# Kernel tuning notes

Measured on AMD Instinct MI355X. Metric: run time of the kernel, lower is better.

## Reference

```python
import jax, jax.numpy as jnp
import numpy as np

B, L, D = 8, 8192, 1024
M = L // 4  # target_ratio=4 -> exactly L/4 boundaries per batch row (enforced in setup_inputs)


@jax.custom_vjp
def ste(x):
    # Forward: ones_like(x). Backward: pass gradient straight through.
    return jnp.ones_like(x)

def _ste_fwd(x):
    return jnp.ones_like(x), None

def _ste_bwd(_, g):
    return (g,)

ste.defvjp(_ste_fwd, _ste_bwd)


def _ema_combine(c1, c2):
    # Linear recurrence h = a*h_prev + b as an associative op (matches the
    # Hillis-Steele doubling scan in the torch source exactly).
    a1, b1 = c1
    a2, b2 = c2
    return (a1 * a2, a2[..., None] * b1 + b2)


def setup_inputs() -> dict:
    key = jax.random.key(0)
    k1, k2, k3, k4, k5 = jax.random.split(key, 5)
    x = jax.random.normal(k1, (B, L, D), jnp.float32)
    residual = jax.random.normal(k2, (B, L, D), jnp.float32)
    prob = jax.random.uniform(k3, (B, L), jnp.float32)
    # exactly M=L//4 True positions per row (random locations) -> static M
    r = jax.random.uniform(k4, (B, L))
    sel = jnp.argsort(r, axis=1)[:, :M]
    token_mask = jnp.zeros((B, L), bool).at[jnp.arange(B)[:, None], sel].set(True)
    state = jax.random.normal(k5, (B, D), jnp.float32)
    return {"x": x, "residual": residual, "prob": prob,
            "token_mask": token_mask, "state": state}


def reference(x, residual, prob, token_mask, state):
    # ---- Tokenizer: compact selected positions to the front (stable order) ----
    counts = token_mask.sum(axis=1)                       # (B,)
    order = jnp.argsort(~token_mask, axis=1)[:, :M]       # stable: True positions first, in order
    chunked = jnp.take_along_axis(x, order[:, :, None], axis=1)      # (B, M, D)
    chunk_probs = jnp.take_along_axis(prob, order, axis=1)           # (B, M)
    valid = jnp.arange(M)[None, :] < counts[:, None]                  # (B, M)
    chunk_probs = chunk_probs * valid                     # padded slots -> 0 (new_zeros semantics)

    # ---- EMA scan over compacted chunks ----
    decay = jnp.clip(1.0 - chunk_probs, 0.0, 1.0)         # (B, M)
    b = (1.0 - decay)[..., None] * chunked                # (B, M, D)
    b = b.at[:, 0].add(decay[:, 0, None] * state)         # fold initial state into b[0]
    _, ema = jax.lax.associative_scan(_ema_combine, (decay, b), axis=1)
    ema = ema * valid[..., None]

    # ---- DeTokenizer: scatter-expand back to (B, L, D) ----
    chunk_idx = jnp.cumsum(token_mask.astype(jnp.int32), axis=1) - 1  # (B, L)
    valid_pos = chunk_idx >= 0
    ci = jnp.clip(chunk_idx, 0, M - 1)
    long_states = jnp.take_along_axis(ema, ci[:, :, None], axis=1)    # (B, L, D)
    long_states = long_states * valid_pos[..., None]

    coef = ste(jnp.maximum(1.0 - prob, prob))             # forward: ones; bwd: STE
    long_states = long_states * coef[..., None]

    output = residual + long_states                       # (B, L, D)

    # new_state = last valid EMA value per batch (or carried-over state if empty)
    last = jnp.clip(counts - 1, 0, M - 1)
    new_state = jnp.take_along_axis(ema, last[:, None, None], axis=1)[:, 0]
    new_state = jnp.where((counts > 0)[:, None], new_state, state)
    return output, new_state
```

## Files before the change

kernel.cpp:

```cpp
#include <hip/hip_runtime.h>
#include <stdint.h>
#include <stddef.h>

#define B_ 8
#define L_ 8192
#define D_ 1024
#define M_ 2048
#define D4_ (D_/4)
#define TROWS_ 256
#define NTILE_ (L_/TROWS_)
#define NBLK_ (B_*NTILE_)

typedef float f4 __attribute__((ext_vector_type(4)));

#define OFF_FLAG   ((size_t)0)
#define OFF_A      ((size_t)256)
#define OFF_CNT    (OFF_A    + (size_t)NBLK_*4)
#define OFF_LIVE   (OFF_CNT  + (size_t)NBLK_*4)
#define OFF_EZ     (OFF_LIVE + (size_t)NBLK_*4)
#define OFF_HINIT  (OFF_EZ   + (size_t)NBLK_*D_*4)
#define WS_TOTAL   (OFF_HINIT + (size_t)NBLK_*D_*4)

__global__ __launch_bounds__(256)
void segend_kernel(const f4* __restrict__ x4,
                   const float* __restrict__ prob,
                   const void* __restrict__ mask_raw,
                   f4* __restrict__ ez4,
                   float* __restrict__ Aseg,
                   int* __restrict__ cnt,
                   int* __restrict__ u8out) {
    const int blk = blockIdx.x;
    const int b = blk >> 5;
    const int k = blk & (NTILE_ - 1);
    const int t = threadIdx.x;
    const int l0 = k * TROWS_;

    __shared__ int   u8flag;
    __shared__ int   wsum[4];
    __shared__ int   pl[TROWS_ + 2];
    __shared__ float dl[TROWS_ + 2];

    if (t == 0) u8flag = 0;
    __syncthreads();
    {
        const uint32_t* mu = (const uint32_t*)mask_raw;
        uint32_t orv = 0;
        #pragma unroll
        for (int j = 0; j < 8; j++) orv |= mu[t * 8 + j];
        if (orv > 1u) atomicOr(&u8flag, 1);
    }
    pl[t] = L_; dl[t] = 1.0f;
    if (t < 2) { pl[TROWS_ + t] = L_; dl[TROWS_ + t] = 1.0f; }
    __syncthreads();
    const bool u8 = (u8flag != 0);
    if (blk == 0 && t == 0) *u8out = u8 ? 1 : 0;

    const int gl = b * L_ + l0 + t;
    const int mv = u8 ? (((const uint8_t*)mask_raw)[gl] ? 1 : 0)
                      : (((const int*)mask_raw)[gl] ? 1 : 0);
    const float dv = fminf(fmaxf(1.0f - prob[gl], 0.0f), 1.0f);
    const int lane = t & 63, wid = t >> 6;
    int v = mv;
    #pragma unroll
    for (int off = 1; off < 64; off <<= 1) {
        int nn = __shfl_up(v, off, 64);
        if (lane >= off) v += nn;
    }
    if (lane == 63) wsum[wid] = v;
    __syncthreads();
    int acc = 0;
    #pragma unroll
    for (int w = 0; w < 4; w++) if (w < wid) acc += wsum[w];
    const int n = wsum[0] + wsum[1] + wsum[2] + wsum[3];
    const int excl = (v - mv) + acc;
    if (mv) { pl[excl] = l0 + t; dl[excl] = dv; }
    __syncthreads();

    f4 h = (f4)(0.0f);
    float A = 1.0f;
    const f4* xrow = x4 + (size_t)b * L_ * D4_;
    for (int g = 0; g < n; g += 8) {
        f4    xv[8];
        float dd[8];
        #pragma unroll
        for (int j = 0; j < 8; j++) {
            const int mm = g + j;
            const int mc = (mm < n) ? mm : 0;
            dd[j] = (mm < n) ? dl[mc] : 1.0f;
            xv[j] = xrow[(size_t)pl[mc] * D4_ + t];
        }
        #pragma unroll
        for (int j = 0; j < 8; j++) {
            h = dd[j] * h + (1.0f - dd[j]) * xv[j];
            A *= dd[j];
        }
    }
    ez4[(size_t)blk * D4_ + t] = h;
    if (t == 0) { Aseg[blk] = A; cnt[blk] = n; }
}

__global__ __launch_bounds__(64)
void combine_kernel(const float* __restrict__ ez,
                    const float* __restrict__ Aseg,
                    const int* __restrict__ cnt,
                    const float* __restrict__ state,
                    float* __restrict__ hinit,
                    int* __restrict__ live,
                    float* __restrict__ newstate) {
    const int b = blockIdx.x;
    const int ch = blockIdx.y * 64 + threadIdx.x;
    __shared__ float Al[NTILE_];
    __shared__ int   Cl[NTILE_];
    if (threadIdx.x < NTILE_) {
        Al[threadIdx.x] = Aseg[b * NTILE_ + threadIdx.x];
        Cl[threadIdx.x] = cnt[b * NTILE_ + threadIdx.x];
    }
    __syncthreads();

    float c = state[(size_t)b * D_ + ch];
    for (int s0 = 0; s0 < NTILE_; s0 += 8) {
        float e[8];
        #pragma unroll
        for (int j = 0; j < 8; j++)
            e[j] = ez[((size_t)b * NTILE_ + s0 + j) * D_ + ch];
        #pragma unroll
        for (int j = 0; j < 8; j++) {
            hinit[((size_t)b * NTILE_ + s0 + j) * D_ + ch] = c;
            c = fmaf(Al[s0 + j], c, e[j]);
        }
    }
    newstate[(size_t)b * D_ + ch] = c;
    if (blockIdx.y == 0 && threadIdx.x == 0) {
        int cc = 0;
        for (int kk = 0; kk < NTILE_; kk++) {
            live[b * NTILE_ + kk] = (cc > 0) ? 1 : 0;
            cc += Cl[kk];
        }
    }
}

__global__ __launch_bounds__(256)
void fused_kernel(const f4* __restrict__ x4,
                  const f4* __restrict__ res4,
                  const float* __restrict__ prob,
                  const void* __restrict__ mask_raw,
                  const int* __restrict__ u8in,
                  const int* __restrict__ liveA,
                  const f4* __restrict__ hinit4,
                  f4* __restrict__ out4) {
    const int blk = blockIdx.x;
    const int b = blk >> 5;
    const int k = blk & (NTILE_ - 1);
    const int t = threadIdx.x;
    const int l0 = k * TROWS_;

    __shared__ int   wsum[4];
    __shared__ int   pl[TROWS_ + 2];
    __shared__ float dl[TROWS_ + 2];

    pl[t] = L_; dl[t] = 1.0f;
    if (t < 2) { pl[TROWS_ + t] = L_; dl[TROWS_ + t] = 1.0f; }
    const bool u8 = (*u8in != 0);

    const int gl = b * L_ + l0 + t;
    const int mv = u8 ? (((const uint8_t*)mask_raw)[gl] ? 1 : 0)
                      : (((const int*)mask_raw)[gl] ? 1 : 0);
    const float dv = fminf(fmaxf(1.0f - prob[gl], 0.0f), 1.0f);
    const int lane = t & 63, wid = t >> 6;
    int v = mv;
    #pragma unroll
    for (int off = 1; off < 64; off <<= 1) {
        int nn = __shfl_up(v, off, 64);
        if (lane >= off) v += nn;
    }
    if (lane == 63) wsum[wid] = v;
    __syncthreads();
    int acc = 0;
    #pragma unroll
    for (int w = 0; w < 4; w++) if (w < wid) acc += wsum[w];
    const int excl = (v - mv) + acc;
    if (mv) { pl[excl] = l0 + t; dl[excl] = dv; }
    __syncthreads();

    const f4* xrow = x4 + (size_t)b * L_ * D4_;

    f4 h = hinit4[(size_t)blk * D4_ + t];
    float live = liveA[blk] ? 1.0f : 0.0f;

    const f4* resrow = res4 + (size_t)b * L_ * D4_;
    f4*       outrow = out4 + (size_t)b * L_ * D4_;

    int mi = 0;
    int nextb = pl[0];
    int a0 = (pl[0] < L_) ? pl[0] : 0;
    int a1 = (pl[1] < L_) ? pl[1] : 0;
    f4 xn  = xrow[(size_t)a0 * D4_ + t];
    f4 xn2 = xrow[(size_t)a1 * D4_ + t];
    int l = l0;

    #define ADV(K, HH, LV)                                                \
        if (l + (K) == nextb) {                                           \
            const float d_ = dl[mi];                                      \
            h = d_ * h + (1.0f - d_) * xn;                                \
            live = 1.0f;                                                  \
            xn = xn2;                                                     \
            ++mi;                                                         \
            nextb = pl[mi];                                               \
            const int nr_ = (pl[mi + 1] < L_) ? pl[mi + 1] : 0;           \
            xn2 = xrow[(size_t)nr_ * D4_ + t];                            \
        }                                                                 \
        HH = h; LV = live;

    #define STORE4                                                        \
        {                                                                 \
            f4 h0, h1, h2, h3;                                            \
            float v0, v1, v2, v3;                                         \
            ADV(0, h0, v0); ADV(1, h1, v1); ADV(2, h2, v2); ADV(3, h3, v3);\
            __builtin_nontemporal_store(c0 + v0 * h0, outrow + (size_t)(l + 0) * D4_ + t); \
            __builtin_nontemporal_store(c1 + v1 * h1, outrow + (size_t)(l + 1) * D4_ + t); \
            __builtin_nontemporal_store(c2 + v2 * h2, outrow + (size_t)(l + 2) * D4_ + t); \
            __builtin_nontemporal_store(c3 + v3 * h3, outrow + (size_t)(l + 3) * D4_ + t); \
        }

    f4 c0 = __builtin_nontemporal_load(resrow + (size_t)(l + 0) * D4_ + t);
    f4 c1 = __builtin_nontemporal_load(resrow + (size_t)(l + 1) * D4_ + t);
    f4 c2 = __builtin_nontemporal_load(resrow + (size_t)(l + 2) * D4_ + t);
    f4 c3 = __builtin_nontemporal_load(resrow + (size_t)(l + 3) * D4_ + t);
    f4 c4 = __builtin_nontemporal_load(resrow + (size_t)(l + 4) * D4_ + t);
    f4 c5 = __builtin_nontemporal_load(resrow + (size_t)(l + 5) * D4_ + t);
    f4 c6 = __builtin_nontemporal_load(resrow + (size_t)(l + 6) * D4_ + t);
    f4 c7 = __builtin_nontemporal_load(resrow + (size_t)(l + 7) * D4_ + t);

    for (int g = 0; g < (TROWS_ / 4) - 2; ++g) {
        f4 n0 = __builtin_nontemporal_load(resrow + (size_t)(l +  8) * D4_ + t);
        f4 n1 = __builtin_nontemporal_load(resrow + (size_t)(l +  9) * D4_ + t);
        f4 n2 = __builtin_nontemporal_load(resrow + (size_t)(l + 10) * D4_ + t);
        f4 n3 = __builtin_nontemporal_load(resrow + (size_t)(l + 11) * D4_ + t);
        STORE4;
        c0 = c4; c1 = c5; c2 = c6; c3 = c7;
        c4 = n0; c5 = n1; c6 = n2; c7 = n3;
        l += 4;
    }
    STORE4;
    c0 = c4; c1 = c5; c2 = c6; c3 = c7;
    l += 4;
    STORE4;
    #undef STORE4
    #undef ADV
}

extern "C" void kernel_launch(void* const* d_in, const int* in_sizes, int n_in,
                              void* d_out, int out_size, void* d_ws, size_t ws_size,
                              hipStream_t stream) {
    const float* x        = (const float*)d_in[0];
    const float* residual = (const float*)d_in[1];
    const float* prob     = (const float*)d_in[2];
    const void*  mask     = d_in[3];
    const float* state    = (const float*)d_in[4];

    float* out       = (float*)d_out;
    float* new_state = out + (size_t)B_ * L_ * D_;

    if (ws_size < WS_TOTAL) return;

    char* ws = (char*)d_ws;
    int*   u8flag = (int*)  (ws + OFF_FLAG);
    float* Aseg   = (float*)(ws + OFF_A);
    int*   cnt    = (int*)  (ws + OFF_CNT);
    int*   live   = (int*)  (ws + OFF_LIVE);
    float* ez     = (float*)(ws + OFF_EZ);
    float* hinit  = (float*)(ws + OFF_HINIT);

    segend_kernel<<<NBLK_, 256, 0, stream>>>(
        (const f4*)x, prob, mask, (f4*)ez, Aseg, cnt, u8flag);

    combine_kernel<<<dim3(B_, 16), 64, 0, stream>>>(
        ez, Aseg, cnt, state, hinit, live, new_state);

    fused_kernel<<<NBLK_, 256, 0, stream>>>(
        (const f4*)x, (const f4*)residual, prob, mask, u8flag, live,
        (const f4*)hinit, (f4*)out);
}
```

Baseline: 120.9 us.

## Fuse cross-tile carry combine into main kernel, drop combine launch

Removes the separate combine kernel. Each block of the fused kernel now recomputes its own initial carry by sequentially combining the preceding tiles' segment-end values, decays and counts, and the last tile writes new_state. This removes one launch plus the hinit/live workspace round-trip, and the combine no longer runs as a tiny serial grid of only 8x16 blocks. In exchange, the redundant prefix work is quadratic in tiles (up to 31 ez reads per thread for later tiles), added before the main loop.

```diff
diff --git a/kernel.cpp b/kernel.cpp
--- a/kernel.cpp
+++ b/kernel.cpp
@@ -16,10 +16,8 @@
 #define OFF_FLAG   ((size_t)0)
 #define OFF_A      ((size_t)256)
 #define OFF_CNT    (OFF_A    + (size_t)NBLK_*4)
-#define OFF_LIVE   (OFF_CNT  + (size_t)NBLK_*4)
-#define OFF_EZ     (OFF_LIVE + (size_t)NBLK_*4)
-#define OFF_HINIT  (OFF_EZ   + (size_t)NBLK_*D_*4)
-#define WS_TOTAL   (OFF_HINIT + (size_t)NBLK_*D_*4)
+#define OFF_EZ     (OFF_CNT  + (size_t)NBLK_*4)
+#define WS_TOTAL   (OFF_EZ   + (size_t)NBLK_*D_*4)
 
 __global__ __launch_bounds__(256)
 void segend_kernel(const f4* __restrict__ x4,
@@ -99,55 +97,18 @@
     if (t == 0) { Aseg[blk] = A; cnt[blk] = n; }
 }
 
-__global__ __launch_bounds__(64)
-void combine_kernel(const float* __restrict__ ez,
-                    const float* __restrict__ Aseg,
-                    const int* __restrict__ cnt,
-                    const float* __restrict__ state,
-                    float* __restrict__ hinit,
-                    int* __restrict__ live,
-                    float* __restrict__ newstate) {
-    const int b = blockIdx.x;
-    const int ch = blockIdx.y * 64 + threadIdx.x;
-    __shared__ float Al[NTILE_];
-    __shared__ int   Cl[NTILE_];
-    if (threadIdx.x < NTILE_) {
-        Al[threadIdx.x] = Aseg[b * NTILE_ + threadIdx.x];
-        Cl[threadIdx.x] = cnt[b * NTILE_ + threadIdx.x];
-    }
-    __syncthreads();
-
-    float c = state[(size_t)b * D_ + ch];
-    for (int s0 = 0; s0 < NTILE_; s0 += 8) {
-        float e[8];
-        #pragma unroll
-        for (int j = 0; j < 8; j++)
-            e[j] = ez[((size_t)b * NTILE_ + s0 + j) * D_ + ch];
-        #pragma unroll
-        for (int j = 0; j < 8; j++) {
-            hinit[((size_t)b * NTILE_ + s0 + j) * D_ + ch] = c;
-            c = fmaf(Al[s0 + j], c, e[j]);
-        }
-    }
-    newstate[(size_t)b * D_ + ch] = c;
-    if (blockIdx.y == 0 && threadIdx.x == 0) {
-        int cc = 0;
-        for (int kk = 0; kk < NTILE_; kk++) {
-            live[b * NTILE_ + kk] = (cc > 0) ? 1 : 0;
-            cc += Cl[kk];
-        }
-    }
-}
-
 __global__ __launch_bounds__(256)
 void fused_kernel(const f4* __restrict__ x4,
                   const f4* __restrict__ res4,
                   const float* __restrict__ prob,
                   const void* __restrict__ mask_raw,
                   const int* __restrict__ u8in,
-                  const int* __restrict__ liveA,
-                  const f4* __restrict__ hinit4,
-                  f4* __restrict__ out4) {
+                  const f4* __restrict__ ez4,
+                  const float* __restrict__ Aseg,
+                  const int* __restrict__ cnt,
+                  const float* __restrict__ state,
+                  f4* __restrict__ out4,
+                  float* __restrict__ newstate) {
     const int blk = blockIdx.x;
     const int b = blk >> 5;
     const int k = blk & (NTILE_ - 1);
@@ -157,9 +118,15 @@
     __shared__ int   wsum[4];
     __shared__ int   pl[TROWS_ + 2];
     __shared__ float dl[TROWS_ + 2];
+    __shared__ float Al[NTILE_];
+    __shared__ int   Cl[NTILE_];
 
     pl[t] = L_; dl[t] = 1.0f;
     if (t < 2) { pl[TROWS_ + t] = L_; dl[TROWS_ + t] = 1.0f; }
+    if (t < NTILE_) {
+        Al[t] = Aseg[b * NTILE_ + t];
+        Cl[t] = cnt[b * NTILE_ + t];
+    }
     const bool u8 = (*u8in != 0);
 
     const int gl = b * L_ + l0 + t;
@@ -180,13 +147,36 @@
     for (int w = 0; w < 4; w++) if (w < wid) acc += wsum[w];
     const int excl = (v - mv) + acc;
     if (mv) { pl[excl] = l0 + t; dl[excl] = dv; }
+
+    const f4* ezrow = ez4 + (size_t)b * NTILE_ * D4_;
+    f4 c = ((const f4*)state)[(size_t)b * D4_ + t];
+    int cc = 0;
+    for (int j0 = 0; j0 < k; j0 += 8) {
+        f4 e[8];
+        #pragma unroll
+        for (int j = 0; j < 8; j++) {
+            const int jj = j0 + j;
+            const int jc = (jj < k) ? jj : 0;
+            e[j] = ezrow[(size_t)jc * D4_ + t];
+        }
+        #pragma unroll
+        for (int j = 0; j < 8; j++) {
+            const int jj = j0 + j;
+            if (jj < k) {
+                c = e[j] + Al[jj] * c;
+                cc += Cl[jj];
+            }
+        }
+    }
+    if (k == NTILE_ - 1) {
+        const f4 cfin = ezrow[(size_t)k * D4_ + t] + Al[k] * c;
+        ((f4*)newstate)[(size_t)b * D4_ + t] = cfin;
+    }
+    f4 h = c;
+    float live = (cc > 0) ? 1.0f : 0.0f;
     __syncthreads();
 
     const f4* xrow = x4 + (size_t)b * L_ * D4_;
-
-    f4 h = hinit4[(size_t)blk * D4_ + t];
-    float live = liveA[blk] ? 1.0f : 0.0f;
-
     const f4* resrow = res4 + (size_t)b * L_ * D4_;
     f4*       outrow = out4 + (size_t)b * L_ * D4_;
 
@@ -267,17 +257,12 @@
     int*   u8flag = (int*)  (ws + OFF_FLAG);
     float* Aseg   = (float*)(ws + OFF_A);
     int*   cnt    = (int*)  (ws + OFF_CNT);
-    int*   live   = (int*)  (ws + OFF_LIVE);
     float* ez     = (float*)(ws + OFF_EZ);
-    float* hinit  = (float*)(ws + OFF_HINIT);
 
     segend_kernel<<<NBLK_, 256, 0, stream>>>(
         (const f4*)x, prob, mask, (f4*)ez, Aseg, cnt, u8flag);
 
-    combine_kernel<<<dim3(B_, 16), 64, 0, stream>>>(
-        ez, Aseg, cnt, state, hinit, live, new_state);
-
     fused_kernel<<<NBLK_, 256, 0, stream>>>(
-        (const f4*)x, (const f4*)residual, prob, mask, u8flag, live,
-        (const f4*)hinit, (f4*)out);
+        (const f4*)x, (const f4*)residual, prob, mask, u8flag,
+        (const f4*)ez, Aseg, cnt, state, (f4*)out, new_state);
 }
```

Measured after the change: 122.7 us. No clear change (+1.4%).
